# Performance work log

Hardware: AMD Instinct MI355X
Metric: run time of the kernel (lower is better)

Reference implementation:

```python
import jax, jax.numpy as jnp
import numpy as np

TEMPERATURE = 0.1  # use_temperature=True


def setup_inputs() -> dict:
    key = jax.random.key(0)
    # encoder output features: [batch_size, num_epoch, feature_dim]
    feature = jax.random.normal(key, (128, 64, 128), dtype=jnp.float32)
    return {"feature": feature}


def reference(feature):
    # L2-normalize along feature dim (F.normalize, p=2, dim=1 on flat features)
    f = feature / jnp.linalg.norm(feature, axis=-1, keepdims=True)
    B, E, D = f.shape
    # full pairwise logits: [B, E, E, B]
    logits = jnp.einsum('ijk,mnk->ijnm', f, f) / TEMPERATURE
    e = jnp.exp(logits)
    idx = jnp.arange(B)
    # mask[i, j, :, i] = 1 -> positives are the m == i block: e[i, j, :, i]
    pos = e[idx, :, :, idx].sum(-1)              # [B, E]
    neg = e.sum(axis=(2, 3)) - pos               # [B, E] everything else
    loss = (-jnp.log(pos / (pos + neg))).mean()
    return loss
```

## Files before the change

### kernel.cpp

```cpp
#include <hip/hip_runtime.h>
#include <hip/hip_bf16.h>

#define N_ROWS 8192
#define DIM    128
#define TILE   128
#define CPG    8
#define EXPTEN 22026.465794806718f
#define SCALE  3.7982826f

typedef __attribute__((ext_vector_type(8))) short short8;
typedef __attribute__((ext_vector_type(4))) float floatx4;

#define EXP2F(x) __builtin_amdgcn_exp2f(x)

__global__ void norm_kernel(const float* __restrict__ F, __hip_bfloat16* __restrict__ Xb,
                            float* __restrict__ pos, float* __restrict__ den) {
    int lane = threadIdx.x & 63;
    int wave = threadIdx.x >> 6;
    int row  = blockIdx.x * 4 + wave;
    const float2 v = *(const float2*)(F + (size_t)row * DIM + lane * 2);
    float ss = v.x * v.x + v.y * v.y;
    #pragma unroll
    for (int m = 1; m < 64; m <<= 1) ss += __shfl_xor(ss, m);
    float inv = rsqrtf(ss) * SCALE;
    __hip_bfloat162 o;
    o.x = __float2bfloat16(v.x * inv);
    o.y = __float2bfloat16(v.y * inv);
    *((__hip_bfloat162*)(Xb + (size_t)row * DIM) + lane) = o;
    if (lane == 0) { pos[row] = 0.f; den[row] = 0.f; }
}

__global__ __launch_bounds__(256, 2) void gram_kernel(
        const __hip_bfloat16* __restrict__ Xb,
        float* __restrict__ pos, float* __restrict__ den) {
    const int tid  = threadIdx.x;
    const int rb   = blockIdx.x;
    const int cg   = blockIdx.y;
    const int lane = tid & 63;
    const int wave = tid >> 6;
    const int wm   = wave >> 1, wn = wave & 1;
    const int quad = lane >> 4;
    const int l15  = lane & 15;

    short8 af[4][4];
    {
        const __hip_bfloat16* Ab = Xb + ((size_t)(rb * TILE + wm * 64 + l15)) * DIM + quad * 8;
        #pragma unroll
        for (int mi = 0; mi < 4; ++mi)
            #pragma unroll
            for (int ko = 0; ko < 4; ++ko)
                af[mi][ko] = *(const short8*)(Ab + mi * 16 * DIM + ko * 32);
    }

    float dp[4][4];
    #pragma unroll
    for (int a = 0; a < 4; ++a)
        #pragma unroll
        for (int b = 0; b < 4; ++b) dp[a][b] = 0.f;

    const __hip_bfloat16* Bb =
        Xb + ((size_t)(cg * CPG * TILE + wn * 64 + l15)) * DIM + quad * 8;

    short8 bq[4][4];
    #pragma unroll
    for (int ni = 0; ni < 4; ++ni)
        #pragma unroll
        for (int ko = 0; ko < 4; ++ko)
            bq[ni][ko] = *(const short8*)(Bb + ni * 16 * DIM + ko * 32);

    auto do_tile = [&](int t, bool refill) {
        const int ct = cg * CPG + t;
        const bool pos_tile = (ct == rb) && (wm == wn);
        const __hip_bfloat16* Bn = Bb + (size_t)(t + 1) * TILE * DIM;

        float dadd[4][4];
        #pragma unroll
        for (int mi = 0; mi < 4; ++mi)
            #pragma unroll
            for (int rg = 0; rg < 4; ++rg) dadd[mi][rg] = 0.f;

        #pragma unroll
        for (int ni = 0; ni < 4; ++ni) {
            floatx4 acc[4];
            #pragma unroll
            for (int mi = 0; mi < 4; ++mi) acc[mi] = (floatx4)0.0f;
            #pragma unroll
            for (int ko = 0; ko < 4; ++ko)
                #pragma unroll
                for (int mi = 0; mi < 4; ++mi)
                    acc[mi] = __builtin_amdgcn_mfma_f32_16x16x32_bf16(
                        af[mi][ko], bq[ni][ko], acc[mi], 0, 0, 0);
            if (refill)
                #pragma unroll
                for (int ko = 0; ko < 4; ++ko)
                    bq[ni][ko] = *(const short8*)(Bn + ni * 16 * DIM + ko * 32);
            #pragma unroll
            for (int mi = 0; mi < 4; ++mi)
                #pragma unroll
                for (int rg = 0; rg < 4; ++rg) {
                    float ex = EXP2F(acc[mi][rg]);
                    if (pos_tile && ni == mi && l15 == quad * 4 + rg)
                        ex = EXPTEN;
                    dadd[mi][rg] += ex;
                }
        }

        #pragma unroll
        for (int mi = 0; mi < 4; ++mi)
            #pragma unroll
            for (int rg = 0; rg < 4; ++rg) {
                if (pos_tile) {
                    float p = dadd[mi][rg];
                    #pragma unroll
                    for (int m = 1; m < 16; m <<= 1) p += __shfl_xor(p, m);
                    if (l15 == 0)
                        atomicAdd(&pos[rb * TILE + wm * 64 + mi * 16 + quad * 4 + rg], p);
                }
                dp[mi][rg] += dadd[mi][rg];
            }
    };

    #pragma unroll 1
    for (int t = 0; t < CPG - 1; ++t)
        do_tile(t, true);
    do_tile(CPG - 1, false);

    #pragma unroll
    for (int mi = 0; mi < 4; ++mi)
        #pragma unroll
        for (int rg = 0; rg < 4; ++rg) {
            float d = dp[mi][rg];
            #pragma unroll
            for (int m = 1; m < 16; m <<= 1) d += __shfl_xor(d, m);
            if (l15 == 0)
                atomicAdd(&den[rb * TILE + wm * 64 + mi * 16 + quad * 4 + rg], d);
        }
}

__global__ void loss_kernel(const float* __restrict__ pos, const float* __restrict__ den,
                            float* __restrict__ out) {
    __shared__ float red[4];
    float acc = 0.f;
    for (int i = threadIdx.x; i < N_ROWS / 4; i += 256) {
        float4 d = ((const float4*)den)[i];
        float4 p = ((const float4*)pos)[i];
        acc += __logf(d.x / p.x) + __logf(d.y / p.y) +
               __logf(d.z / p.z) + __logf(d.w / p.w);
    }
    #pragma unroll
    for (int m = 1; m < 64; m <<= 1) acc += __shfl_xor(acc, m);
    int lane = threadIdx.x & 63, w = threadIdx.x >> 6;
    if (lane == 0) red[w] = acc;
    __syncthreads();
    if (threadIdx.x == 0)
        out[0] = (red[0] + red[1] + red[2] + red[3]) * (1.0f / (float)N_ROWS);
}

extern "C" void kernel_launch(void* const* d_in, const int* in_sizes, int n_in,
                              void* d_out, int out_size, void* d_ws, size_t ws_size,
                              hipStream_t stream) {
    const float* feature = (const float*)d_in[0];
    float* pos = (float*)d_ws;
    float* den = pos + N_ROWS;
    __hip_bfloat16* Xb = (__hip_bfloat16*)(den + N_ROWS);

    norm_kernel<<<N_ROWS / 4, 256, 0, stream>>>(feature, Xb, pos, den);
    gram_kernel<<<dim3(64, N_ROWS / TILE / CPG), 256, 0, stream>>>(Xb, pos, den);
    loss_kernel<<<1, 256, 0, stream>>>(pos, den, (float*)d_out);
}
```

Baseline: 98.97 us.

## Stage column block in swizzled LDS and reuse it across several row blocks

The gram kernel now loads a 256-column B block once into LDS with direct global-to-LDS loads and an XOR swizzle. Each workgroup then loops over 4 row blocks against it, reloading only the A fragments from global memory. Before, every workgroup streamed 8 column tiles from global into registers. The intent is to cut global/L2 traffic for B and improve reuse. In exchange it uses 64KB of LDS per block, which may limit occupancy, adds LDS read latency in the inner loop, and splits den atomics into one per row block.

```diff
diff --git a/kernel.cpp b/kernel.cpp
--- a/kernel.cpp
+++ b/kernel.cpp
@@ -4,7 +4,8 @@
 #define N_ROWS 8192
 #define DIM    128
 #define TILE   128
-#define CPG    8
+#define BCOLS  256
+#define RPB    4
 #define EXPTEN 22026.465794806718f
 #define SCALE  3.7982826f
 
@@ -12,6 +13,11 @@
 typedef __attribute__((ext_vector_type(4))) float floatx4;
 
 #define EXP2F(x) __builtin_amdgcn_exp2f(x)
+
+#define GLOAD_LDS(g, l)                                                        \
+    __builtin_amdgcn_global_load_lds(                                          \
+        (const __attribute__((address_space(1))) void*)(g),                    \
+        (__attribute__((address_space(3))) void*)(l), 16, 0, 0)
 
 __global__ void norm_kernel(const float* __restrict__ F, __hip_bfloat16* __restrict__ Xb,
                             float* __restrict__ pos, float* __restrict__ den) {
@@ -33,8 +39,9 @@
 __global__ __launch_bounds__(256, 2) void gram_kernel(
         const __hip_bfloat16* __restrict__ Xb,
         float* __restrict__ pos, float* __restrict__ den) {
+    __shared__ __hip_bfloat16 Bs[BCOLS * DIM];
     const int tid  = threadIdx.x;
-    const int rb   = blockIdx.x;
+    const int rbg  = blockIdx.x;
     const int cg   = blockIdx.y;
     const int lane = tid & 63;
     const int wave = tid >> 6;
@@ -42,8 +49,19 @@
     const int quad = lane >> 4;
     const int l15  = lane & 15;
 
+    #pragma unroll
+    for (int it = 0; it < 16; ++it) {
+        int chunk = (it * 4 + wave) * 64 + lane;
+        int r  = chunk >> 4;
+        int cs = (chunk & 15) ^ (r & 15);
+        const __hip_bfloat16* gp = Xb + ((size_t)(cg * BCOLS + r)) * DIM + cs * 8;
+        char* lp = (char*)&Bs[0] + (it * 4 + wave) * 1024;
+        GLOAD_LDS(gp, lp);
+    }
+
     short8 af[4][4];
     {
+        const int rb = rbg * RPB;
         const __hip_bfloat16* Ab = Xb + ((size_t)(rb * TILE + wm * 64 + l15)) * DIM + quad * 8;
         #pragma unroll
         for (int mi = 0; mi < 4; ++mi)
@@ -51,36 +69,31 @@
             for (int ko = 0; ko < 4; ++ko)
                 af[mi][ko] = *(const short8*)(Ab + mi * 16 * DIM + ko * 32);
     }
+    __syncthreads();
 
-    float dp[4][4];
-    #pragma unroll
-    for (int a = 0; a < 4; ++a)
+    const char* Bw = (const char*)&Bs[0] + (size_t)wn * 128 * 256;
+
+    #pragma unroll 1
+    for (int rbi = 0; rbi < RPB; ++rbi) {
+        const int rb = rbg * RPB + rbi;
+        const int dlt = (rb * 2 + wm) - (cg * 4 + wn * 2);
+        const bool has_pos = (dlt == 0) || (dlt == 1);
+
+        float dp[4][4], pp[4][4];
         #pragma unroll
-        for (int b = 0; b < 4; ++b) dp[a][b] = 0.f;
-
-    const __hip_bfloat16* Bb =
-        Xb + ((size_t)(cg * CPG * TILE + wn * 64 + l15)) * DIM + quad * 8;
-
-    short8 bq[4][4];
-    #pragma unroll
-    for (int ni = 0; ni < 4; ++ni)
-        #pragma unroll
-        for (int ko = 0; ko < 4; ++ko)
-            bq[ni][ko] = *(const short8*)(Bb + ni * 16 * DIM + ko * 32);
-
-    auto do_tile = [&](int t, bool refill) {
-        const int ct = cg * CPG + t;
-        const bool pos_tile = (ct == rb) && (wm == wn);
-        const __hip_bfloat16* Bn = Bb + (size_t)(t + 1) * TILE * DIM;
-
-        float dadd[4][4];
-        #pragma unroll
-        for (int mi = 0; mi < 4; ++mi)
+        for (int a = 0; a < 4; ++a)
             #pragma unroll
-            for (int rg = 0; rg < 4; ++rg) dadd[mi][rg] = 0.f;
+            for (int b = 0; b < 4; ++b) { dp[a][b] = 0.f; pp[a][b] = 0.f; }
 
         #pragma unroll
-        for (int ni = 0; ni < 4; ++ni) {
+        for (int ni = 0; ni < 8; ++ni) {
+            short8 bf[4];
+            #pragma unroll
+            for (int ko = 0; ko < 4; ++ko) {
+                int r  = ni * 16 + l15;
+                int ch = (ko * 4 + quad) ^ l15;
+                bf[ko] = *(const short8*)(Bw + r * 256 + ch * 16);
+            }
             floatx4 acc[4];
             #pragma unroll
             for (int mi = 0; mi < 4; ++mi) acc[mi] = (floatx4)0.0f;
@@ -89,52 +102,55 @@
                 #pragma unroll
                 for (int mi = 0; mi < 4; ++mi)
                     acc[mi] = __builtin_amdgcn_mfma_f32_16x16x32_bf16(
-                        af[mi][ko], bq[ni][ko], acc[mi], 0, 0, 0);
-            if (refill)
-                #pragma unroll
-                for (int ko = 0; ko < 4; ++ko)
-                    bq[ni][ko] = *(const short8*)(Bn + ni * 16 * DIM + ko * 32);
+                        af[mi][ko], bf[ko], acc[mi], 0, 0, 0);
+
+            const bool posni = has_pos && ((ni >> 2) == dlt);
+            const int  nl    = ni & 3;
             #pragma unroll
             for (int mi = 0; mi < 4; ++mi)
                 #pragma unroll
                 for (int rg = 0; rg < 4; ++rg) {
                     float ex = EXP2F(acc[mi][rg]);
-                    if (pos_tile && ni == mi && l15 == quad * 4 + rg)
+                    if (posni && nl == mi && l15 == quad * 4 + rg)
                         ex = EXPTEN;
-                    dadd[mi][rg] += ex;
+                    dp[mi][rg] += ex;
+                    if (posni) pp[mi][rg] += ex;
                 }
+        }
+
+        if (rbi + 1 < RPB) {
+            const __hip_bfloat16* Ab =
+                Xb + ((size_t)((rb + 1) * TILE + wm * 64 + l15)) * DIM + quad * 8;
+            #pragma unroll
+            for (int mi = 0; mi < 4; ++mi)
+                #pragma unroll
+                for (int ko = 0; ko < 4; ++ko)
+                    af[mi][ko] = *(const short8*)(Ab + mi * 16 * DIM + ko * 32);
         }
 
         #pragma unroll
         for (int mi = 0; mi < 4; ++mi)
             #pragma unroll
             for (int rg = 0; rg < 4; ++rg) {
-                if (pos_tile) {
-                    float p = dadd[mi][rg];
+                float d = dp[mi][rg];
+                #pragma unroll
+                for (int m = 1; m < 16; m <<= 1) d += __shfl_xor(d, m);
+                if (l15 == 0)
+                    atomicAdd(&den[rb * TILE + wm * 64 + mi * 16 + quad * 4 + rg], d);
+            }
+        if (has_pos) {
+            #pragma unroll
+            for (int mi = 0; mi < 4; ++mi)
+                #pragma unroll
+                for (int rg = 0; rg < 4; ++rg) {
+                    float p = pp[mi][rg];
                     #pragma unroll
                     for (int m = 1; m < 16; m <<= 1) p += __shfl_xor(p, m);
                     if (l15 == 0)
                         atomicAdd(&pos[rb * TILE + wm * 64 + mi * 16 + quad * 4 + rg], p);
                 }
-                dp[mi][rg] += dadd[mi][rg];
-            }
-    };
-
-    #pragma unroll 1
-    for (int t = 0; t < CPG - 1; ++t)
-        do_tile(t, true);
-    do_tile(CPG - 1, false);
-
-    #pragma unroll
-    for (int mi = 0; mi < 4; ++mi)
-        #pragma unroll
-        for (int rg = 0; rg < 4; ++rg) {
-            float d = dp[mi][rg];
-            #pragma unroll
-            for (int m = 1; m < 16; m <<= 1) d += __shfl_xor(d, m);
-            if (l15 == 0)
-                atomicAdd(&den[rb * TILE + wm * 64 + mi * 16 + quad * 4 + rg], d);
         }
+    }
 }
 
 __global__ void loss_kernel(const float* __restrict__ pos, const float* __restrict__ den,
@@ -165,6 +181,6 @@
     __hip_bfloat16* Xb = (__hip_bfloat16*)(den + N_ROWS);
 
     norm_kernel<<<N_ROWS / 4, 256, 0, stream>>>(feature, Xb, pos, den);
-    gram_kernel<<<dim3(64, N_ROWS / TILE / CPG), 256, 0, stream>>>(Xb, pos, den);
+    gram_kernel<<<dim3(N_ROWS / TILE / RPB, N_ROWS / BCOLS), 256, 0, stream>>>(Xb, pos, den);
     loss_kernel<<<1, 256, 0, stream>>>(pos, den, (float*)d_out);
 }
```

Result: slower. 124.6 us (+25.9%).
